# Optimization experiments

Hardware: AMD Instinct MI355X
Metric: run time of the kernel (lower is better)

Reference implementation:

```python
import jax, jax.numpy as jnp
import numpy as np

N_NODES = 25000
N_EDGES = 400000
N = 2          # per-node group dim (h.size(1))
IN_DIM = 64
HEADS = 4
HEAD_DIM = 16  # out_dim; HEADS*HEAD_DIM == IN_DIM here


def setup_inputs() -> dict:
    key = jax.random.key(0)
    ks = jax.random.split(key, 8)
    w_scale = 1.0 / np.sqrt(IN_DIM)
    return {
        "h": jax.random.normal(ks[0], (N_NODES, N, IN_DIM), jnp.float32),
        "e": jax.random.normal(ks[1], (N_EDGES, N, IN_DIM), jnp.float32),
        "W_Q": jax.random.normal(ks[2], (IN_DIM, HEADS * HEAD_DIM), jnp.float32) * w_scale,
        "W_K": jax.random.normal(ks[3], (IN_DIM, HEADS * HEAD_DIM), jnp.float32) * w_scale,
        "W_V": jax.random.normal(ks[4], (IN_DIM, HEADS * HEAD_DIM), jnp.float32) * w_scale,
        "W_repe": jax.random.normal(ks[5], (IN_DIM, HEADS * HEAD_DIM), jnp.float32) * w_scale,
        "src": jax.random.randint(ks[6], (N_EDGES,), 0, N_NODES, jnp.int32),
        "dst": jax.random.randint(ks[7], (N_EDGES,), 0, N_NODES, jnp.int32),
    }


def reference(h, e, W_Q, W_K, W_V, W_repe, src, dst):
    n_nodes, Nd, C = h.shape
    E = src.shape[0]
    # node-side projection Q_h: [n_nodes, N, H, D]
    Q_h = (h @ W_Q).reshape(n_nodes, Nd, HEADS, HEAD_DIM)
    # edge-side bias repe_e: [E, N, H, D]
    repe_e = (e @ W_repe).reshape(E, Nd, HEADS, HEAD_DIM)
    # compute_diff: relu(src - dst) on raw features  [E, N, C]
    diff = jax.nn.relu(h[src] - h[dst])
    k_diff = (diff @ W_K).reshape(E, Nd, HEADS, HEAD_DIM)
    v_diff = (diff @ W_V).reshape(E, Nd, HEADS, HEAD_DIM)
    # dst_cosim_diff: scale = ||k_diff|| * ||Q_h[dst]|| + 1e-6 (norm over last dim, keepdim)
    q_dst = Q_h[dst]  # [E, N, H, D]
    scale = (jnp.linalg.norm(k_diff, axis=-1, keepdims=True)
             * jnp.linalg.norm(q_dst, axis=-1, keepdims=True)) + 1e-6
    score = q_dst * k_diff * scale + repe_e
    msg = score * v_diff
    # update_all(copy_edge, max) -> segment max over dst; zero-degree nodes get 0 (DGL convention)
    h_out = jax.ops.segment_max(msg, dst, num_segments=n_nodes)
    h_out = jnp.where(jnp.isneginf(h_out), jnp.zeros((), h_out.dtype), h_out)
    return h_out
```

## Files before the change

kernel.cpp:

```cpp
#include <hip/hip_runtime.h>
#include <stdint.h>

#define N_NODES 25000
#define N_EDGES 400000

typedef __attribute__((ext_vector_type(8))) short short8;
typedef __attribute__((ext_vector_type(4))) short short4v;
typedef __attribute__((ext_vector_type(4))) float f32x4;

#define MFMA16(a, b, c) __builtin_amdgcn_mfma_f32_16x16x32_bf16((a), (b), (c), 0, 0, 0)

__device__ __forceinline__ short bf16r(float x) {
    unsigned u = __float_as_uint(x);
    u += 0x7FFFu + ((u >> 16) & 1u);
    return (short)(u >> 16);
}

__device__ __forceinline__ short8 load_bfrag(const float* __restrict__ W,
                                             int colbase, int lane, int khalf) {
    const int n = colbase + (lane & 15);
    const int k0 = khalf * 32 + ((lane >> 4) << 3);
    short8 f;
    #pragma unroll
    for (int j = 0; j < 8; ++j) f[j] = bf16r(W[(k0 + j) * 64 + n]);
    return f;
}

__device__ __forceinline__ short8 afrag(const short* S, int lane, int khalf) {
    return *(const short8*)&S[(lane & 15) * 72 + khalf * 32 + ((lane >> 4) << 3)];
}

__global__ __launch_bounds__(256) void zero_counts_kernel(int* __restrict__ counts) {
    const int i = blockIdx.x * 256 + threadIdx.x;
    if (i < N_NODES) counts[i] = 0;
}

__global__ __launch_bounds__(256) void hist_kernel(const int* __restrict__ dst,
                                                   int* __restrict__ counts) {
    const int i = blockIdx.x * 256 + threadIdx.x;
    if (i < N_EDGES) atomicAdd(&counts[dst[i]], 1);
}

#define BPT 98
__global__ __launch_bounds__(256) void scan_kernel(const int* __restrict__ counts,
                                                   int* __restrict__ offsets,
                                                   int* __restrict__ cursor) {
    __shared__ int part[256];
    const int t = threadIdx.x;
    const int base = t * BPT;
    int s = 0;
    for (int j = 0; j < BPT; ++j) {
        const int idx = base + j;
        if (idx < N_NODES) s += counts[idx];
    }
    part[t] = s;
    __syncthreads();
    for (int d = 1; d < 256; d <<= 1) {
        const int add = (t >= d) ? part[t - d] : 0;
        __syncthreads();
        part[t] += add;
        __syncthreads();
    }
    int run = (t > 0) ? part[t - 1] : 0;
    for (int j = 0; j < BPT; ++j) {
        const int idx = base + j;
        if (idx < N_NODES) {
            offsets[idx] = run;
            cursor[idx]  = run;
            run += counts[idx];
        }
    }
    if (t == 255) offsets[N_NODES] = part[255];
}

__global__ __launch_bounds__(256) void scatter_kernel(
    const int* __restrict__ src, const int* __restrict__ dst,
    int* __restrict__ cursor, int* __restrict__ perm, int* __restrict__ srcs) {
    const int i = blockIdx.x * 256 + threadIdx.x;
    if (i < N_EDGES) {
        const int d = dst[i];
        const int pos = atomicAdd(&cursor[d], 1);
        perm[pos] = i;
        srcs[pos] = src[i];
    }
}

__global__ __launch_bounds__(256) void prep_frag_kernel(
    const float* __restrict__ Wk, const float* __restrict__ Wv,
    const float* __restrict__ Wr, short8* __restrict__ fw) {
    const int t = threadIdx.x;
    const int w = t >> 6, lane = t & 63, wcol = w << 4;
    fw[(w * 6 + 0) * 64 + lane] = load_bfrag(Wk, wcol, lane, 0);
    fw[(w * 6 + 1) * 64 + lane] = load_bfrag(Wk, wcol, lane, 1);
    fw[(w * 6 + 2) * 64 + lane] = load_bfrag(Wv, wcol, lane, 0);
    fw[(w * 6 + 3) * 64 + lane] = load_bfrag(Wv, wcol, lane, 1);
    fw[(w * 6 + 4) * 64 + lane] = load_bfrag(Wr, wcol, lane, 0);
    fw[(w * 6 + 5) * 64 + lane] = load_bfrag(Wr, wcol, lane, 1);
}

__global__ __launch_bounds__(256) void q_mfma_kernel(
    const float* __restrict__ h, const float* __restrict__ Wq, float* __restrict__ Q)
{
    __shared__ short sH[64 * 72];
    const int t = threadIdx.x;
    const int lane = t & 63, w = t >> 6;
    const int wcol = w << 4;
    const int ln = lane & 15, lq = lane >> 4;
    const int base = blockIdx.x * 64;

    const short8 b0 = load_bfrag(Wq, wcol, lane, 0);
    const short8 b1 = load_bfrag(Wq, wcol, lane, 1);

    {
        const int r = t >> 2, c4 = (t & 3) << 4;
        int row = base + r; if (row > 49999) row = 49999;
        const float4* p = (const float4*)&h[row * 64 + c4];
        short tmp[16];
        #pragma unroll
        for (int i = 0; i < 4; ++i) {
            float4 x = p[i];
            tmp[4*i+0] = bf16r(x.x); tmp[4*i+1] = bf16r(x.y);
            tmp[4*i+2] = bf16r(x.z); tmp[4*i+3] = bf16r(x.w);
        }
        *(short8*)&sH[r * 72 + c4]     = *(short8*)&tmp[0];
        *(short8*)&sH[r * 72 + c4 + 8] = *(short8*)&tmp[8];
    }
    __syncthreads();

    #pragma unroll
    for (int m = 0; m < 4; ++m) {
        const short* Sm = &sH[(m << 4) * 72];
        short8 a0 = afrag(Sm, lane, 0);
        short8 a1 = afrag(Sm, lane, 1);
        f32x4 acc = {0.f, 0.f, 0.f, 0.f};
        acc = MFMA16(a0, b0, acc);
        acc = MFMA16(a1, b1, acc);
        #pragma unroll
        for (int reg = 0; reg < 4; ++reg) {
            const int row = base + (m << 4) + (lq << 2) + reg;
            if (row < 50000) Q[row * 64 + wcol + ln] = acc[reg];
        }
    }
}

__global__ __launch_bounds__(256) void edge_csr_kernel(
    const float* __restrict__ h, const float* __restrict__ e,
    const float* __restrict__ Q, const int* __restrict__ srcs,
    const int* __restrict__ perm, const int* __restrict__ offsets,
    const short8* __restrict__ fw, float* __restrict__ out)
{
    const int v = blockIdx.x;
    const int t = threadIdx.x;
    const int off0 = offsets[v], off1 = offsets[v + 1];
    const int deg = off1 - off0;
    if (deg == 0) {
        if (t < 128) out[(v << 7) + t] = 0.0f;
        return;
    }
    __shared__ short sD[16 * 72];
    __shared__ short sE[16 * 72];
    const int lane = t & 63, w = t >> 6;
    const int wcol = w << 4;
    const int ln = lane & 15, lq = lane >> 4;

    const short8 bK0 = fw[(w * 6 + 0) * 64 + lane];
    const short8 bK1 = fw[(w * 6 + 1) * 64 + lane];
    const short8 bV0 = fw[(w * 6 + 2) * 64 + lane];
    const short8 bV1 = fw[(w * 6 + 3) * 64 + lane];
    const short8 bR0 = fw[(w * 6 + 4) * 64 + lane];
    const short8 bR1 = fw[(w * 6 + 5) * 64 + lane];

    const float q0 = Q[((v << 1) + 0) * 64 + wcol + ln];
    const float q1 = Q[((v << 1) + 1) * 64 + wcol + ln];
    float s0 = q0 * q0, s1 = q1 * q1;
    s0 += __shfl_xor(s0, 1); s1 += __shfl_xor(s1, 1);
    s0 += __shfl_xor(s0, 2); s1 += __shfl_xor(s1, 2);
    s0 += __shfl_xor(s0, 4); s1 += __shfl_xor(s1, 4);
    s0 += __shfl_xor(s0, 8); s1 += __shfl_xor(s1, 8);
    const float qn0 = sqrtf(s0), qn1 = sqrtf(s1);

    const float NEG_INF = __uint_as_float(0xFF800000u);
    float rm0 = NEG_INF, rm1 = NEG_INF;

    const int r = t >> 4;
    const int cq = (t & 15) << 2;
    const int n_r = r & 1;
    const int hd_base = (((v << 1) + n_r) << 6);

    const int nchunks = (deg + 7) >> 3;
    for (int c = 0; c < nchunks; ++c) {
        {
            int eidx = off0 + (c << 3) + (r >> 1);
            const int ec = (eidx < off1 - 1) ? eidx : (off1 - 1);
            const int ed = perm[ec];
            const int s  = srcs[ec];
            const float4 xs = *(const float4*)&h[((((s  << 1) + n_r) << 6)) + cq];
            const float4 xd = *(const float4*)&h[hd_base + cq];
            const float4 xe = *(const float4*)&e[((((ed << 1) + n_r) << 6)) + cq];
            short4v d4, e4;
            d4[0] = bf16r(fmaxf(xs.x - xd.x, 0.f));
            d4[1] = bf16r(fmaxf(xs.y - xd.y, 0.f));
            d4[2] = bf16r(fmaxf(xs.z - xd.z, 0.f));
            d4[3] = bf16r(fmaxf(xs.w - xd.w, 0.f));
            e4[0] = bf16r(xe.x); e4[1] = bf16r(xe.y);
            e4[2] = bf16r(xe.z); e4[3] = bf16r(xe.w);
            *(short4v*)&sD[r * 72 + cq] = d4;
            *(short4v*)&sE[r * 72 + cq] = e4;
        }
        __syncthreads();

        short8 a0 = afrag(sD, lane, 0);
        short8 a1 = afrag(sD, lane, 1);
        short8 g0 = afrag(sE, lane, 0);
        short8 g1 = afrag(sE, lane, 1);
        f32x4 aK = {0.f, 0.f, 0.f, 0.f}, aV = aK, aR = aK;
        aK = MFMA16(a0, bK0, aK); aK = MFMA16(a1, bK1, aK);
        aV = MFMA16(a0, bV0, aV); aV = MFMA16(a1, bV1, aV);
        aR = MFMA16(g0, bR0, aR); aR = MFMA16(g1, bR1, aR);

        #pragma unroll
        for (int reg = 0; reg < 4; ++reg) {
            const int rl = (lq << 2) + reg;
            const int eloc = rl >> 1;
            const bool valid = ((c << 3) + eloc) < deg;
            const float kk = aK[reg];
            float sk = kk * kk;
            sk += __shfl_xor(sk, 1);
            sk += __shfl_xor(sk, 2);
            sk += __shfl_xor(sk, 4);
            sk += __shfl_xor(sk, 8);
            const int n2 = rl & 1;
            const float scale = sqrtf(sk) * (n2 ? qn1 : qn0) + 1e-6f;
            const float qv = n2 ? q1 : q0;
            float msg = (qv * kk * scale + aR[reg]) * aV[reg];
            msg = valid ? msg : NEG_INF;
            if (n2) rm1 = fmaxf(rm1, msg); else rm0 = fmaxf(rm0, msg);
        }
        __syncthreads();
    }

    rm0 = fmaxf(rm0, __shfl_xor(rm0, 16));
    rm0 = fmaxf(rm0, __shfl_xor(rm0, 32));
    rm1 = fmaxf(rm1, __shfl_xor(rm1, 16));
    rm1 = fmaxf(rm1, __shfl_xor(rm1, 32));
    if (lq == 0) out[(v << 7) + wcol + ln]      = rm0;
    if (lq == 1) out[(v << 7) + 64 + wcol + ln] = rm1;
}

extern "C" void kernel_launch(void* const* d_in, const int* in_sizes, int n_in,
                              void* d_out, int out_size, void* d_ws, size_t ws_size,
                              hipStream_t stream) {
    const float* h  = (const float*)d_in[0];
    const float* e  = (const float*)d_in[1];
    const float* Wq = (const float*)d_in[2];
    const float* Wk = (const float*)d_in[3];
    const float* Wv = (const float*)d_in[4];
    const float* Wr = (const float*)d_in[5];
    const int*   src = (const int*)d_in[6];
    const int*   dst = (const int*)d_in[7];
    float* out = (float*)d_out;

    float* Q       = (float*)d_ws;
    int*   counts  = (int*)d_ws + 3200000;
    int*   offsets = (int*)d_ws + 3225000;
    int*   cursor  = (int*)d_ws + 3250008;
    int*   perm    = (int*)d_ws + 3275008;
    int*   srcs    = (int*)d_ws + 3675008;
    short8* fw     = (short8*)((int*)d_ws + 4075008);

    zero_counts_kernel<<<98, 256, 0, stream>>>(counts);
    hist_kernel<<<1563, 256, 0, stream>>>(dst, counts);
    scan_kernel<<<1, 256, 0, stream>>>(counts, offsets, cursor);
    scatter_kernel<<<1563, 256, 0, stream>>>(src, dst, cursor, perm, srcs);
    prep_frag_kernel<<<1, 256, 0, stream>>>(Wk, Wv, Wr, fw);
    q_mfma_kernel<<<782, 256, 0, stream>>>(h, Wq, Q);
    edge_csr_kernel<<<25000, 256, 0, stream>>>(h, e, Q, srcs, perm, offsets, fw, out);
}
```

Before: 526.7 us.

## Process one destination node per wave instead of per block

The edge kernel now assigns one destination node to each wavefront, with four nodes per block. Each wave computes all four heads with MFMA, and the block-wide __syncthreads becomes a wave barrier with per-wave shared memory. The weight-fragment prep is folded into the Q projection kernel, removing one launch. Row reductions use DPP adds instead of shuffles, and bf16 conversion uses a cheaper round-half-up in place of round-to-nearest-even, which slightly changes numerics. The changes aim to cut barrier and launch overhead and idle threads on low-degree nodes, at the cost of more registers per lane and possible load imbalance within a block.

```diff
diff --git a/kernel.cpp b/kernel.cpp
--- a/kernel.cpp
+++ b/kernel.cpp
@@ -5,7 +5,6 @@
 #define N_EDGES 400000
 
 typedef __attribute__((ext_vector_type(8))) short short8;
-typedef __attribute__((ext_vector_type(4))) short short4v;
 typedef __attribute__((ext_vector_type(4))) float f32x4;
 
 #define MFMA16(a, b, c) __builtin_amdgcn_mfma_f32_16x16x32_bf16((a), (b), (c), 0, 0, 0)
@@ -14,6 +13,19 @@
     unsigned u = __float_as_uint(x);
     u += 0x7FFFu + ((u >> 16) & 1u);
     return (short)(u >> 16);
+}
+__device__ __forceinline__ short bfr(float x) {
+    return (short)((__float_as_uint(x) + 0x8000u) >> 16);
+}
+
+#define DPP_ADD(x, ctrl) \
+    ((x) + __int_as_float(__builtin_amdgcn_update_dpp(0, __float_as_int(x), (ctrl), 0xF, 0xF, true)))
+__device__ __forceinline__ float red16(float x) {
+    x = DPP_ADD(x, 0xB1);
+    x = DPP_ADD(x, 0x4E);
+    x = DPP_ADD(x, 0x141);
+    x = DPP_ADD(x, 0x140);
+    return x;
 }
 
 __device__ __forceinline__ short8 load_bfrag(const float* __restrict__ W,
@@ -85,21 +97,10 @@
     }
 }
 
-__global__ __launch_bounds__(256) void prep_frag_kernel(
+__global__ __launch_bounds__(256) void q_mfma_kernel(
+    const float* __restrict__ h, const float* __restrict__ Wq,
     const float* __restrict__ Wk, const float* __restrict__ Wv,
-    const float* __restrict__ Wr, short8* __restrict__ fw) {
-    const int t = threadIdx.x;
-    const int w = t >> 6, lane = t & 63, wcol = w << 4;
-    fw[(w * 6 + 0) * 64 + lane] = load_bfrag(Wk, wcol, lane, 0);
-    fw[(w * 6 + 1) * 64 + lane] = load_bfrag(Wk, wcol, lane, 1);
-    fw[(w * 6 + 2) * 64 + lane] = load_bfrag(Wv, wcol, lane, 0);
-    fw[(w * 6 + 3) * 64 + lane] = load_bfrag(Wv, wcol, lane, 1);
-    fw[(w * 6 + 4) * 64 + lane] = load_bfrag(Wr, wcol, lane, 0);
-    fw[(w * 6 + 5) * 64 + lane] = load_bfrag(Wr, wcol, lane, 1);
-}
-
-__global__ __launch_bounds__(256) void q_mfma_kernel(
-    const float* __restrict__ h, const float* __restrict__ Wq, float* __restrict__ Q)
+    const float* __restrict__ Wr, float* __restrict__ Q, short8* __restrict__ fw)
 {
     __shared__ short sH[64 * 72];
     const int t = threadIdx.x;
@@ -141,110 +142,145 @@
             if (row < 50000) Q[row * 64 + wcol + ln] = acc[reg];
         }
     }
-}
-
-__global__ __launch_bounds__(256) void edge_csr_kernel(
+
+    if (blockIdx.x == 0) {
+        fw[(w * 6 + 0) * 64 + lane] = load_bfrag(Wk, wcol, lane, 0);
+        fw[(w * 6 + 1) * 64 + lane] = load_bfrag(Wk, wcol, lane, 1);
+        fw[(w * 6 + 2) * 64 + lane] = load_bfrag(Wv, wcol, lane, 0);
+        fw[(w * 6 + 3) * 64 + lane] = load_bfrag(Wv, wcol, lane, 1);
+        fw[(w * 6 + 4) * 64 + lane] = load_bfrag(Wr, wcol, lane, 0);
+        fw[(w * 6 + 5) * 64 + lane] = load_bfrag(Wr, wcol, lane, 1);
+    }
+}
+
+__global__ __launch_bounds__(256, 2) void edge_wave_kernel(
     const float* __restrict__ h, const float* __restrict__ e,
     const float* __restrict__ Q, const int* __restrict__ srcs,
     const int* __restrict__ perm, const int* __restrict__ offsets,
     const short8* __restrict__ fw, float* __restrict__ out)
 {
-    const int v = blockIdx.x;
+    __shared__ short sAll[4][2304];
     const int t = threadIdx.x;
-    const int off0 = offsets[v], off1 = offsets[v + 1];
-    const int deg = off1 - off0;
+    const int lane = t & 63, w = t >> 6;
+    const int v = (blockIdx.x << 2) + w;
+    short* SD = &sAll[w][0];
+    short* SE = &sAll[w][1152];
+
+    const int off0 = offsets[v];
+    const int off1 = offsets[v + 1];
+    const int deg  = off1 - off0;
+
     if (deg == 0) {
-        if (t < 128) out[(v << 7) + t] = 0.0f;
+        out[(v << 7) + lane]      = 0.0f;
+        out[(v << 7) + 64 + lane] = 0.0f;
         return;
     }
-    __shared__ short sD[16 * 72];
-    __shared__ short sE[16 * 72];
-    const int lane = t & 63, w = t >> 6;
-    const int wcol = w << 4;
+
     const int ln = lane & 15, lq = lane >> 4;
 
-    const short8 bK0 = fw[(w * 6 + 0) * 64 + lane];
-    const short8 bK1 = fw[(w * 6 + 1) * 64 + lane];
-    const short8 bV0 = fw[(w * 6 + 2) * 64 + lane];
-    const short8 bV1 = fw[(w * 6 + 3) * 64 + lane];
-    const short8 bR0 = fw[(w * 6 + 4) * 64 + lane];
-    const short8 bR1 = fw[(w * 6 + 5) * 64 + lane];
-
-    const float q0 = Q[((v << 1) + 0) * 64 + wcol + ln];
-    const float q1 = Q[((v << 1) + 1) * 64 + wcol + ln];
-    float s0 = q0 * q0, s1 = q1 * q1;
-    s0 += __shfl_xor(s0, 1); s1 += __shfl_xor(s1, 1);
-    s0 += __shfl_xor(s0, 2); s1 += __shfl_xor(s1, 2);
-    s0 += __shfl_xor(s0, 4); s1 += __shfl_xor(s1, 4);
-    s0 += __shfl_xor(s0, 8); s1 += __shfl_xor(s1, 8);
-    const float qn0 = sqrtf(s0), qn1 = sqrtf(s1);
+    short8 bK0[4], bK1[4], bV0[4], bV1[4], bR0[4], bR1[4];
+    #pragma unroll
+    for (int hd = 0; hd < 4; ++hd) {
+        bK0[hd] = fw[(hd * 6 + 0) * 64 + lane];
+        bK1[hd] = fw[(hd * 6 + 1) * 64 + lane];
+        bV0[hd] = fw[(hd * 6 + 2) * 64 + lane];
+        bV1[hd] = fw[(hd * 6 + 3) * 64 + lane];
+        bR0[hd] = fw[(hd * 6 + 4) * 64 + lane];
+        bR1[hd] = fw[(hd * 6 + 5) * 64 + lane];
+    }
+
+    float q0[4], q1[4], qn0[4], qn1[4];
+    #pragma unroll
+    for (int hd = 0; hd < 4; ++hd) {
+        q0[hd] = Q[(v << 7) + (hd << 4) + ln];
+        q1[hd] = Q[(v << 7) + 64 + (hd << 4) + ln];
+        qn0[hd] = sqrtf(red16(q0[hd] * q0[hd]));
+        qn1[hd] = sqrtf(red16(q1[hd] * q1[hd]));
+    }
+
+    const int r = lane >> 2;
+    const int cq = (lane & 3) << 4;
+    const int n_r = r & 1;
+
+    float4 xd[4];
+    {
+        const float4* pd = (const float4*)&h[(((v << 1) + n_r) << 6) + cq];
+        xd[0] = pd[0]; xd[1] = pd[1]; xd[2] = pd[2]; xd[3] = pd[3];
+    }
 
     const float NEG_INF = __uint_as_float(0xFF800000u);
-    float rm0 = NEG_INF, rm1 = NEG_INF;
-
-    const int r = t >> 4;
-    const int cq = (t & 15) << 2;
-    const int n_r = r & 1;
-    const int hd_base = (((v << 1) + n_r) << 6);
-
-    const int nchunks = (deg + 7) >> 3;
-    for (int c = 0; c < nchunks; ++c) {
-        {
-            int eidx = off0 + (c << 3) + (r >> 1);
-            const int ec = (eidx < off1 - 1) ? eidx : (off1 - 1);
-            const int ed = perm[ec];
-            const int s  = srcs[ec];
-            const float4 xs = *(const float4*)&h[((((s  << 1) + n_r) << 6)) + cq];
-            const float4 xd = *(const float4*)&h[hd_base + cq];
-            const float4 xe = *(const float4*)&e[((((ed << 1) + n_r) << 6)) + cq];
-            short4v d4, e4;
-            d4[0] = bf16r(fmaxf(xs.x - xd.x, 0.f));
-            d4[1] = bf16r(fmaxf(xs.y - xd.y, 0.f));
-            d4[2] = bf16r(fmaxf(xs.z - xd.z, 0.f));
-            d4[3] = bf16r(fmaxf(xs.w - xd.w, 0.f));
-            e4[0] = bf16r(xe.x); e4[1] = bf16r(xe.y);
-            e4[2] = bf16r(xe.z); e4[3] = bf16r(xe.w);
-            *(short4v*)&sD[r * 72 + cq] = d4;
-            *(short4v*)&sE[r * 72 + cq] = e4;
-        }
-        __syncthreads();
-
-        short8 a0 = afrag(sD, lane, 0);
-        short8 a1 = afrag(sD, lane, 1);
-        short8 g0 = afrag(sE, lane, 0);
-        short8 g1 = afrag(sE, lane, 1);
-        f32x4 aK = {0.f, 0.f, 0.f, 0.f}, aV = aK, aR = aK;
-        aK = MFMA16(a0, bK0, aK); aK = MFMA16(a1, bK1, aK);
-        aV = MFMA16(a0, bV0, aV); aV = MFMA16(a1, bV1, aV);
-        aR = MFMA16(g0, bR0, aR); aR = MFMA16(g1, bR1, aR);
-
+    float rm0[4] = {NEG_INF, NEG_INF, NEG_INF, NEG_INF};
+    float rm1[4] = {NEG_INF, NEG_INF, NEG_INF, NEG_INF};
+
+    const int nch = (deg + 7) >> 3;
+    for (int c = 0; c < nch; ++c) {
+        int eidx = off0 + (c << 3) + (r >> 1);
+        if (eidx > off1 - 1) eidx = off1 - 1;
+        const int ed = perm[eidx];
+        const int s  = srcs[eidx];
+        const float4* ps = (const float4*)&h[(((s  << 1) + n_r) << 6) + cq];
+        const float4* pe = (const float4*)&e[(((ed << 1) + n_r) << 6) + cq];
+
+        short tmd[16], tme[16];
         #pragma unroll
-        for (int reg = 0; reg < 4; ++reg) {
-            const int rl = (lq << 2) + reg;
-            const int eloc = rl >> 1;
-            const bool valid = ((c << 3) + eloc) < deg;
-            const float kk = aK[reg];
-            float sk = kk * kk;
-            sk += __shfl_xor(sk, 1);
-            sk += __shfl_xor(sk, 2);
-            sk += __shfl_xor(sk, 4);
-            sk += __shfl_xor(sk, 8);
-            const int n2 = rl & 1;
-            const float scale = sqrtf(sk) * (n2 ? qn1 : qn0) + 1e-6f;
-            const float qv = n2 ? q1 : q0;
-            float msg = (qv * kk * scale + aR[reg]) * aV[reg];
-            msg = valid ? msg : NEG_INF;
-            if (n2) rm1 = fmaxf(rm1, msg); else rm0 = fmaxf(rm0, msg);
-        }
-        __syncthreads();
-    }
-
-    rm0 = fmaxf(rm0, __shfl_xor(rm0, 16));
-    rm0 = fmaxf(rm0, __shfl_xor(rm0, 32));
-    rm1 = fmaxf(rm1, __shfl_xor(rm1, 16));
-    rm1 = fmaxf(rm1, __shfl_xor(rm1, 32));
-    if (lq == 0) out[(v << 7) + wcol + ln]      = rm0;
-    if (lq == 1) out[(v << 7) + 64 + wcol + ln] = rm1;
+        for (int i = 0; i < 4; ++i) {
+            const float4 xs = ps[i], xe = pe[i];
+            tmd[4*i+0] = bfr(fmaxf(xs.x - xd[i].x, 0.f));
+            tmd[4*i+1] = bfr(fmaxf(xs.y - xd[i].y, 0.f));
+            tmd[4*i+2] = bfr(fmaxf(xs.z - xd[i].z, 0.f));
+            tmd[4*i+3] = bfr(fmaxf(xs.w - xd[i].w, 0.f));
+            tme[4*i+0] = bfr(xe.x); tme[4*i+1] = bfr(xe.y);
+            tme[4*i+2] = bfr(xe.z); tme[4*i+3] = bfr(xe.w);
+        }
+        *(short8*)&SD[r * 72 + cq]     = *(short8*)&tmd[0];
+        *(short8*)&SD[r * 72 + cq + 8] = *(short8*)&tmd[8];
+        *(short8*)&SE[r * 72 + cq]     = *(short8*)&tme[0];
+        *(short8*)&SE[r * 72 + cq + 8] = *(short8*)&tme[8];
+
+        __builtin_amdgcn_wave_barrier();
+
+        const short8 a0 = afrag(SD, lane, 0);
+        const short8 a1 = afrag(SD, lane, 1);
+        const short8 g0 = afrag(SE, lane, 0);
+        const short8 g1 = afrag(SE, lane, 1);
+
+        #pragma unroll
+        for (int hd = 0; hd < 4; ++hd) {
+            f32x4 aK = {0.f, 0.f, 0.f, 0.f}, aV = aK, aR = aK;
+            aK = MFMA16(a0, bK0[hd], aK); aK = MFMA16(a1, bK1[hd], aK);
+            aV = MFMA16(a0, bV0[hd], aV); aV = MFMA16(a1, bV1[hd], aV);
+            aR = MFMA16(g0, bR0[hd], aR); aR = MFMA16(g1, bR1[hd], aR);
+
+            #pragma unroll
+            for (int reg = 0; reg < 4; ++reg) {
+                const int rl   = (lq << 2) + reg;
+                const int eloc = rl >> 1;
+                const int n2   = reg & 1;
+                const bool valid = ((c << 3) + eloc) < deg;
+                const float kk = aK[reg];
+                const float sk = red16(kk * kk);
+                const float scale = sqrtf(sk) * (n2 ? qn1[hd] : qn0[hd]) + 1e-6f;
+                const float qv = n2 ? q1[hd] : q0[hd];
+                float msg = (qv * kk * scale + aR[reg]) * aV[reg];
+                msg = valid ? msg : NEG_INF;
+                if (n2) rm1[hd] = fmaxf(rm1[hd], msg);
+                else    rm0[hd] = fmaxf(rm0[hd], msg);
+            }
+        }
+        __builtin_amdgcn_wave_barrier();
+    }
+
+    #pragma unroll
+    for (int hd = 0; hd < 4; ++hd) {
+        rm0[hd] = fmaxf(rm0[hd], __shfl_xor(rm0[hd], 16));
+        rm0[hd] = fmaxf(rm0[hd], __shfl_xor(rm0[hd], 32));
+        rm1[hd] = fmaxf(rm1[hd], __shfl_xor(rm1[hd], 16));
+        rm1[hd] = fmaxf(rm1[hd], __shfl_xor(rm1[hd], 32));
+    }
+    const float o0 = (lq == 0) ? rm0[0] : (lq == 1) ? rm0[1] : (lq == 2) ? rm0[2] : rm0[3];
+    const float o1 = (lq == 0) ? rm1[0] : (lq == 1) ? rm1[1] : (lq == 2) ? rm1[2] : rm1[3];
+    out[(v << 7) + lane]      = o0;
+    out[(v << 7) + 64 + lane] = o1;
 }
 
 extern "C" void kernel_launch(void* const* d_in, const int* in_sizes, int n_in,
@@ -272,7 +308,6 @@
     hist_kernel<<<1563, 256, 0, stream>>>(dst, counts);
     scan_kernel<<<1, 256, 0, stream>>>(counts, offsets, cursor);
     scatter_kernel<<<1563, 256, 0, stream>>>(src, dst, cursor, perm, srcs);
-    prep_frag_kernel<<<1, 256, 0, stream>>>(Wk, Wv, Wr, fw);
-    q_mfma_kernel<<<782, 256, 0, stream>>>(h, Wq, Q);
-    edge_csr_kernel<<<25000, 256, 0, stream>>>(h, e, Q, srcs, perm, offsets, fw, out);
-}
+    q_mfma_kernel<<<782, 256, 0, stream>>>(h, Wq, Wk, Wv, Wr, Q, fw);
+    edge_wave_kernel<<<6250, 256, 0, stream>>>(h, e, Q, srcs, perm, offsets, fw, out);
+}
```

After: 513.4 us. 1.03x faster.
